# Optimization experiments

Hardware: AMD Instinct MI355X
Metric: run time of the kernel (lower is better)

The kernel has to match this reference:

```python
import jax, jax.numpy as jnp
import numpy as np
from jax import lax

WINDOW_SIZE = 11
SIGMA = 1.5
C1 = 0.01 ** 2
C2 = 0.03 ** 2


def _gaussian_window(window_size: int, sigma: float) -> jnp.ndarray:
    coords = jnp.arange(window_size, dtype=jnp.float32) - window_size // 2
    g = jnp.exp(-0.5 * (coords / sigma) ** 2)
    g = g / g.sum()
    return g[:, None] * g[None, :]  # (ws, ws)


def _dwconv(x, win2d):
    # x: (B, C, H, W); win2d: (ws, ws). Depthwise conv, same padding.
    c = x.shape[1]
    ws = win2d.shape[0]
    pad = ws // 2
    k = jnp.broadcast_to(win2d[None, None], (c, 1, ws, ws))  # (O=C, I/g=1, ws, ws)
    return lax.conv_general_dilated(
        x, k, window_strides=(1, 1), padding=[(pad, pad), (pad, pad)],
        dimension_numbers=('NCHW', 'OIHW', 'NCHW'), feature_group_count=c)


def setup_inputs() -> dict:
    key = jax.random.key(0)
    k1, k2 = jax.random.split(key)
    shape = (32, 3, 512, 512)
    img1 = jax.random.uniform(k1, shape, dtype=jnp.float32)
    img2 = jax.random.uniform(k2, shape, dtype=jnp.float32)
    return {"img1": img1, "img2": img2}


def reference(img1, img2):
    win = _gaussian_window(WINDOW_SIZE, SIGMA).astype(img1.dtype)
    mu1 = _dwconv(img1, win)
    mu2 = _dwconv(img2, win)
    mu1_sq = mu1 * mu1
    mu2_sq = mu2 * mu2
    mu12 = mu1 * mu2
    sigma1_sq = _dwconv(img1 * img1, win) - mu1_sq
    sigma2_sq = _dwconv(img2 * img2, win) - mu2_sq
    sigma12 = _dwconv(img1 * img2, win) - mu12
    numerator = (2.0 * mu12 + C1) * (2.0 * sigma12 + C2)
    denominator = (mu1_sq + mu2_sq + C1) * (sigma1_sq + sigma2_sq + C2)
    ssim_map = numerator / denominator
    return 1.0 - ssim_map.mean()
```

## Files before the change

### kernel.cpp

```cpp
#include <hip/hip_runtime.h>

#define IMG   512
#define TW    32
#define TH    32
#define HALO  5
#define WS    11
#define IHH   (TH + 2*HALO)
#define NP    96
#define NSLOT 256

__device__ __constant__ float const_dummy;

__global__ __launch_bounds__(256, 8) void ssim_main(const float* __restrict__ img1,
                                                    const float* __restrict__ img2,
                                                    double* __restrict__ acc) {
    constexpr float W[WS] = {
        0.00102837990674f, 0.00759883148699f, 0.03600079242909f,
        0.10936069869137f, 0.21300538108707f, 0.26601190869814f,
        0.21300538108707f, 0.10936069869137f, 0.03600079242909f,
        0.00759883148699f, 0.00102837990674f };

    __shared__ float hA[5][IHH * TW];

    const int tid = threadIdx.x;
    const int bx = blockIdx.x;
    const int by = blockIdx.y;
    const float* p1 = img1 + (size_t)blockIdx.z * IMG * IMG;
    const float* p2 = img2 + (size_t)blockIdx.z * IMG * IMG;

    for (int u = tid; u < IHH * 8; u += 256) {
        const int r  = u >> 3;
        const int ch = u & 7;
        const int gy = by * TH + r - HALO;
        const bool rowOK = (unsigned)gy < IMG;
        const float* r1 = p1 + (size_t)gy * IMG;
        const float* r2 = p2 + (size_t)gy * IMG;

        float a1[4]  = {0.f,0.f,0.f,0.f};
        float a2[4]  = {0.f,0.f,0.f,0.f};
        float a11[4] = {0.f,0.f,0.f,0.f};
        float a22[4] = {0.f,0.f,0.f,0.f};
        float a12[4] = {0.f,0.f,0.f,0.f};

        #pragma unroll
        for (int j = 0; j < 5; ++j) {
            const int gx = bx * TW + ch * 4 - 8 + 4 * j;
            float4 A = make_float4(0.f,0.f,0.f,0.f), B = A;
            if (rowOK && (unsigned)gx < IMG) {
                A = *(const float4*)(r1 + gx);
                B = *(const float4*)(r2 + gx);
            }
            const float e1[4] = {A.x, A.y, A.z, A.w};
            const float e2[4] = {B.x, B.y, B.z, B.w};
            #pragma unroll
            for (int e = 0; e < 4; ++e) {
                const int i = 4*j + e;
                const float x1 = e1[e], x2 = e2[e];
                const float q11 = x1*x1, q22 = x2*x2, q12 = x1*x2;
                #pragma unroll
                for (int o = 0; o < 4; ++o) {
                    const int t = i - 3 - o;
                    if (t >= 0 && t < WS) {
                        a1[o]  += W[t]*x1;  a2[o]  += W[t]*x2;
                        a11[o] += W[t]*q11; a22[o] += W[t]*q22; a12[o] += W[t]*q12;
                    }
                }
            }
        }

        const int wd = (ch * 4) ^ ((r & 7) << 2);
        float* dst = &hA[0][r * TW + wd];
        const int ss = IHH * TW;
        *(float4*)(dst)        = make_float4(a1[0],a1[1],a1[2],a1[3]);
        *(float4*)(dst + ss)   = make_float4(a2[0],a2[1],a2[2],a2[3]);
        *(float4*)(dst + 2*ss) = make_float4(a11[0],a11[1],a11[2],a11[3]);
        *(float4*)(dst + 3*ss) = make_float4(a22[0],a22[1],a22[2],a22[3]);
        *(float4*)(dst + 4*ss) = make_float4(a12[0],a12[1],a12[2],a12[3]);
    }
    __syncthreads();

    const float C1 = 0.01f*0.01f, C2 = 0.03f*0.03f;
    float lsum = 0.f;
    {
        const int c  = tid & 31;
        const int r0 = (tid >> 5) << 2;
        float m1[4]  = {0.f,0.f,0.f,0.f};
        float m2[4]  = {0.f,0.f,0.f,0.f};
        float m11[4] = {0.f,0.f,0.f,0.f};
        float m22[4] = {0.f,0.f,0.f,0.f};
        float m12[4] = {0.f,0.f,0.f,0.f};

        #pragma unroll
        for (int k = 0; k < 14; ++k) {
            const int row = r0 + k;
            const int off = row * TW + (c ^ ((row & 7) << 2));
            const float h1  = hA[0][off];
            const float h2  = hA[1][off];
            const float h11 = hA[2][off];
            const float h22 = hA[3][off];
            const float h12 = hA[4][off];
            #pragma unroll
            for (int o = 0; o < 4; ++o) {
                const int t = k - o;
                if (t >= 0 && t < WS) {
                    m1[o]  += W[t]*h1;  m2[o]  += W[t]*h2;
                    m11[o] += W[t]*h11; m22[o] += W[t]*h22; m12[o] += W[t]*h12;
                }
            }
        }

        #pragma unroll
        for (int o = 0; o < 4; ++o) {
            const float mu1 = m1[o], mu2 = m2[o];
            const float mu1s = mu1*mu1, mu2s = mu2*mu2, mu12 = mu1*mu2;
            const float s11 = m11[o] - mu1s;
            const float s22 = m22[o] - mu2s;
            const float s12 = m12[o] - mu12;
            const float num = (2.f*mu12 + C1) * (2.f*s12 + C2);
            const float den = (mu1s + mu2s + C1) * (s11 + s22 + C2);
            lsum += num / den;
        }
    }

    #pragma unroll
    for (int d = 32; d >= 1; d >>= 1)
        lsum += __shfl_down(lsum, d, 64);
    __shared__ float wsum[4];
    if ((tid & 63) == 0) wsum[tid >> 6] = lsum;
    __syncthreads();
    if (tid == 0) {
        const float t = wsum[0] + wsum[1] + wsum[2] + wsum[3];
        const int slot = (blockIdx.z * 256 + blockIdx.y * 16 + blockIdx.x) & (NSLOT - 1);
        atomicAdd(&acc[slot], (double)t);
    }
}

__global__ void ssim_final(const double* __restrict__ acc, float* __restrict__ out) {
    const int l = threadIdx.x;
    double s = acc[l] + acc[l + 64] + acc[l + 128] + acc[l + 192];
    #pragma unroll
    for (int d = 32; d >= 1; d >>= 1)
        s += __shfl_down(s, d, 64);
    if (l == 0)
        out[0] = 1.0f - (float)(s / (double)((size_t)NP * IMG * IMG));
}

extern "C" void kernel_launch(void* const* d_in, const int* in_sizes, int n_in,
                              void* d_out, int out_size, void* d_ws, size_t ws_size,
                              hipStream_t stream) {
    const float* img1 = (const float*)d_in[0];
    const float* img2 = (const float*)d_in[1];
    float* out = (float*)d_out;
    double* acc = (double*)d_ws;

    hipMemsetAsync(d_ws, 0, NSLOT * sizeof(double), stream);

    dim3 grid(IMG / TW, IMG / TH, NP);
    ssim_main<<<grid, dim3(256), 0, stream>>>(img1, img2, acc);
    ssim_final<<<1, dim3(64), 0, stream>>>(acc, out);
}
```

Measured before the change: 131.0 us.

## Widen horizontal pass to 8 outputs per thread, pad LDS rows, restructure vertical pass

```diff
diff --git a/kernel.cpp b/kernel.cpp
--- a/kernel.cpp
+++ b/kernel.cpp
@@ -5,13 +5,13 @@
 #define TH    32
 #define HALO  5
 #define WS    11
-#define IHH   (TH + 2*HALO)
+#define IHH   42
+#define LDW   36
+#define SIGSZ (IHH*LDW)
 #define NP    96
 #define NSLOT 256
 
-__device__ __constant__ float const_dummy;
-
-__global__ __launch_bounds__(256, 8) void ssim_main(const float* __restrict__ img1,
+__global__ __launch_bounds__(256, 5) void ssim_main(const float* __restrict__ img1,
                                                     const float* __restrict__ img2,
                                                     double* __restrict__ acc) {
     constexpr float W[WS] = {
@@ -20,45 +20,44 @@
         0.21300538108707f, 0.10936069869137f, 0.03600079242909f,
         0.00759883148699f, 0.00102837990674f };
 
-    __shared__ float hA[5][IHH * TW];
+    __shared__ float hA[5 * SIGSZ];
 
     const int tid = threadIdx.x;
     const int bx = blockIdx.x;
     const int by = blockIdx.y;
-    const float* p1 = img1 + (size_t)blockIdx.z * IMG * IMG;
-    const float* p2 = img2 + (size_t)blockIdx.z * IMG * IMG;
+    const float* p1 = img1 + (size_t)blockIdx.z * (IMG*IMG);
+    const float* p2 = img2 + (size_t)blockIdx.z * (IMG*IMG);
 
-    for (int u = tid; u < IHH * 8; u += 256) {
-        const int r  = u >> 3;
-        const int ch = u & 7;
+    if (tid < IHH * 4) {
+        const int r  = tid >> 2;
+        const int ch = tid & 3;
         const int gy = by * TH + r - HALO;
         const bool rowOK = (unsigned)gy < IMG;
         const float* r1 = p1 + (size_t)gy * IMG;
         const float* r2 = p2 + (size_t)gy * IMG;
 
-        float a1[4]  = {0.f,0.f,0.f,0.f};
-        float a2[4]  = {0.f,0.f,0.f,0.f};
-        float a11[4] = {0.f,0.f,0.f,0.f};
-        float a22[4] = {0.f,0.f,0.f,0.f};
-        float a12[4] = {0.f,0.f,0.f,0.f};
+        float a1[8], a2[8], a11[8], a22[8], a12[8];
+        #pragma unroll
+        for (int o = 0; o < 8; ++o) { a1[o]=0.f; a2[o]=0.f; a11[o]=0.f; a22[o]=0.f; a12[o]=0.f; }
 
         #pragma unroll
-        for (int j = 0; j < 5; ++j) {
-            const int gx = bx * TW + ch * 4 - 8 + 4 * j;
+        for (int j = 0; j < 6; ++j) {
+            const int gx = bx * TW + ch * 8 - 8 + 4 * j;
             float4 A = make_float4(0.f,0.f,0.f,0.f), B = A;
             if (rowOK && (unsigned)gx < IMG) {
                 A = *(const float4*)(r1 + gx);
                 B = *(const float4*)(r2 + gx);
             }
-            const float e1[4] = {A.x, A.y, A.z, A.w};
-            const float e2[4] = {B.x, B.y, B.z, B.w};
+            const float e1[4] = {A.x,A.y,A.z,A.w};
+            const float e2[4] = {B.x,B.y,B.z,B.w};
             #pragma unroll
             for (int e = 0; e < 4; ++e) {
                 const int i = 4*j + e;
+                if (i < 3 || i > 20) continue;
                 const float x1 = e1[e], x2 = e2[e];
                 const float q11 = x1*x1, q22 = x2*x2, q12 = x1*x2;
                 #pragma unroll
-                for (int o = 0; o < 4; ++o) {
+                for (int o = 0; o < 8; ++o) {
                     const int t = i - 3 - o;
                     if (t >= 0 && t < WS) {
                         a1[o]  += W[t]*x1;  a2[o]  += W[t]*x2;
@@ -68,58 +67,66 @@
             }
         }
 
-        const int wd = (ch * 4) ^ ((r & 7) << 2);
-        float* dst = &hA[0][r * TW + wd];
-        const int ss = IHH * TW;
-        *(float4*)(dst)        = make_float4(a1[0],a1[1],a1[2],a1[3]);
-        *(float4*)(dst + ss)   = make_float4(a2[0],a2[1],a2[2],a2[3]);
-        *(float4*)(dst + 2*ss) = make_float4(a11[0],a11[1],a11[2],a11[3]);
-        *(float4*)(dst + 3*ss) = make_float4(a22[0],a22[1],a22[2],a22[3]);
-        *(float4*)(dst + 4*ss) = make_float4(a12[0],a12[1],a12[2],a12[3]);
+        const int wb = r * LDW + ch * 8;
+        *(float4*)&hA[0*SIGSZ + wb]     = make_float4(a1[0],a1[1],a1[2],a1[3]);
+        *(float4*)&hA[0*SIGSZ + wb + 4] = make_float4(a1[4],a1[5],a1[6],a1[7]);
+        *(float4*)&hA[1*SIGSZ + wb]     = make_float4(a2[0],a2[1],a2[2],a2[3]);
+        *(float4*)&hA[1*SIGSZ + wb + 4] = make_float4(a2[4],a2[5],a2[6],a2[7]);
+        *(float4*)&hA[2*SIGSZ + wb]     = make_float4(a11[0],a11[1],a11[2],a11[3]);
+        *(float4*)&hA[2*SIGSZ + wb + 4] = make_float4(a11[4],a11[5],a11[6],a11[7]);
+        *(float4*)&hA[3*SIGSZ + wb]     = make_float4(a22[0],a22[1],a22[2],a22[3]);
+        *(float4*)&hA[3*SIGSZ + wb + 4] = make_float4(a22[4],a22[5],a22[6],a22[7]);
+        *(float4*)&hA[4*SIGSZ + wb]     = make_float4(a12[0],a12[1],a12[2],a12[3]);
+        *(float4*)&hA[4*SIGSZ + wb + 4] = make_float4(a12[4],a12[5],a12[6],a12[7]);
     }
     __syncthreads();
 
-    const float C1 = 0.01f*0.01f, C2 = 0.03f*0.03f;
-    float lsum = 0.f;
-    {
-        const int c  = tid & 31;
-        const int r0 = (tid >> 5) << 2;
-        float m1[4]  = {0.f,0.f,0.f,0.f};
-        float m2[4]  = {0.f,0.f,0.f,0.f};
-        float m11[4] = {0.f,0.f,0.f,0.f};
-        float m22[4] = {0.f,0.f,0.f,0.f};
-        float m12[4] = {0.f,0.f,0.f,0.f};
+    const int c  = tid & 31;
+    const int r0 = (tid >> 5) << 2;
+    float m[5][4];
+    #pragma unroll
+    for (int s = 0; s < 5; ++s)
+        #pragma unroll
+        for (int o = 0; o < 4; ++o) m[s][o] = 0.f;
 
+    #pragma unroll
+    for (int s = 0; s < 5; ++s) {
+        int off = s * SIGSZ + r0 * LDW + c;
+        asm("" : "+v"(off));
         #pragma unroll
-        for (int k = 0; k < 14; ++k) {
-            const int row = r0 + k;
-            const int off = row * TW + (c ^ ((row & 7) << 2));
-            const float h1  = hA[0][off];
-            const float h2  = hA[1][off];
-            const float h11 = hA[2][off];
-            const float h22 = hA[3][off];
-            const float h12 = hA[4][off];
+        for (int k = 0; k < 8; ++k) {
+            const float h = hA[off + k * LDW];
             #pragma unroll
             for (int o = 0; o < 4; ++o) {
                 const int t = k - o;
-                if (t >= 0 && t < WS) {
-                    m1[o]  += W[t]*h1;  m2[o]  += W[t]*h2;
-                    m11[o] += W[t]*h11; m22[o] += W[t]*h22; m12[o] += W[t]*h12;
-                }
+                if (t >= 0 && t < WS) m[s][o] += W[t] * h;
             }
         }
+        int off2 = off + 8 * LDW;
+        asm("" : "+v"(off2));
+        #pragma unroll
+        for (int k = 8; k < 14; ++k) {
+            const float h = hA[off2 + (k - 8) * LDW];
+            #pragma unroll
+            for (int o = 0; o < 4; ++o) {
+                const int t = k - o;
+                if (t >= 0 && t < WS) m[s][o] += W[t] * h;
+            }
+        }
+    }
 
-        #pragma unroll
-        for (int o = 0; o < 4; ++o) {
-            const float mu1 = m1[o], mu2 = m2[o];
-            const float mu1s = mu1*mu1, mu2s = mu2*mu2, mu12 = mu1*mu2;
-            const float s11 = m11[o] - mu1s;
-            const float s22 = m22[o] - mu2s;
-            const float s12 = m12[o] - mu12;
-            const float num = (2.f*mu12 + C1) * (2.f*s12 + C2);
-            const float den = (mu1s + mu2s + C1) * (s11 + s22 + C2);
-            lsum += num / den;
-        }
+    const float C1 = 0.01f*0.01f, C2 = 0.03f*0.03f;
+    float lsum = 0.f;
+    #pragma unroll
+    for (int o = 0; o < 4; ++o) {
+        const float mu1 = m[0][o], mu2 = m[1][o];
+        const float mu1s = mu1*mu1, mu2s = mu2*mu2, mu12 = mu1*mu2;
+        const float s11 = m[2][o] - mu1s;
+        const float s22 = m[3][o] - mu2s;
+        const float s12 = m[4][o] - mu12;
+        const float num = (2.f*mu12 + C1) * (2.f*s12 + C2);
+        const float den = (mu1s + mu2s + C1) * (s11 + s22 + C2);
+        lsum += num * __builtin_amdgcn_rcpf(den);
     }
 
     #pragma unroll
```

Result: faster. 116.4 us (-11.2%).
